# Performance work log

Measured on AMD Instinct MI355X. Metric: run time of the kernel, lower is better.

Reference implementation:

```python
import jax, jax.numpy as jnp
import numpy as np

N, E, B = 100000, 200000, 4096
D, FEAT, L = 300, 512, 5
NUM_ATOM, NUM_CHI = 119, 3
NUM_BOND, NUM_DIR = 5, 3
EPS = 1e-5


def setup_inputs() -> dict:
    key = jax.random.key(0)
    ks = jax.random.split(key, 24)
    x = jax.random.randint(ks[0], (N, 2), 0, 3, dtype=jnp.int32)
    edge_index = jax.random.randint(ks[1], (2, E), 0, N, dtype=jnp.int32)
    edge_attr = jax.random.randint(ks[2], (E, 2), 0, 3, dtype=jnp.int32)
    batch = jnp.sort(jax.random.randint(ks[3], (N,), 0, B, dtype=jnp.int32))
    s = 0.02
    p = {
        'x_emb1': jax.random.normal(ks[4], (NUM_ATOM, D)) * s,
        'x_emb2': jax.random.normal(ks[5], (NUM_CHI, D)) * s,
        'edge_emb1': jax.random.normal(ks[6], (L, NUM_BOND, D)) * s,
        'edge_emb2': jax.random.normal(ks[7], (L, NUM_DIR, D)) * s,
        'W1': jax.random.normal(ks[8], (L, D, 2 * D)) * s,
        'b1': jnp.zeros((L, 2 * D)),
        'W2': jax.random.normal(ks[9], (L, 2 * D, D)) * s,
        'b2': jnp.zeros((L, D)),
        'gamma': jnp.ones((L, D)),
        'beta': jnp.zeros((L, D)),
        'W_feat': jax.random.normal(ks[10], (D, FEAT)) * s,
        'b_feat': jnp.zeros((FEAT,)),
        'Wp1': jax.random.normal(ks[11], (FEAT, FEAT // 2)) * s,
        'bp1': jnp.zeros((FEAT // 2,)),
        'Wp2': jax.random.normal(ks[12], (FEAT // 2, FEAT // 2)) * s,
        'bp2': jnp.zeros((FEAT // 2,)),
        'Wp3': jax.random.normal(ks[13], (FEAT // 2, 2)) * s,
        'bp3': jnp.zeros((2,)),
    }
    return dict(x=x, edge_index=edge_index, edge_attr=edge_attr, batch=batch, **p)


def reference(x, edge_index, edge_attr, batch, x_emb1, x_emb2, edge_emb1, edge_emb2,
              W1, b1, W2, b2, gamma, beta, W_feat, b_feat, Wp1, bp1, Wp2, bp2, Wp3, bp3):
    n = x.shape[0]
    ar = jnp.arange(n, dtype=edge_index.dtype)
    src = jnp.concatenate([edge_index[0], ar])  # [E+N] message sources
    dst = jnp.concatenate([edge_index[1], ar])  # [E+N] aggregation targets
    # self-loop edge attr: bond type 4, direction 0
    sl = jnp.stack([jnp.full((n,), 4, edge_attr.dtype), jnp.zeros((n,), edge_attr.dtype)], axis=1)
    ea = jnp.concatenate([edge_attr, sl], axis=0)  # [E+N, 2]

    h = x_emb1[x[:, 0]] + x_emb2[x[:, 1]]  # [N, D]
    for l in range(L):
        ee = edge_emb1[l][ea[:, 0]] + edge_emb2[l][ea[:, 1]]  # [E+N, D]
        msg = h[src] + ee
        aggr = jax.ops.segment_sum(msg, dst, num_segments=n)  # GIN add-aggregate
        h = jax.nn.relu(aggr @ W1[l] + b1[l]) @ W2[l] + b2[l]
        mu = h.mean(axis=0)
        var = ((h - mu) ** 2).mean(axis=0)  # biased var (torch BN training mode)
        h = (h - mu) * jax.lax.rsqrt(var + EPS) * gamma[l] + beta[l]
        if l < L - 1:
            h = jax.nn.relu(h)

    ones = jnp.ones((n,), h.dtype)
    counts = jax.ops.segment_sum(ones, batch, num_segments=B)
    pooled = jax.ops.segment_sum(h, batch, num_segments=B) / jnp.maximum(counts, 1.0)[:, None]
    hf = pooled @ W_feat + b_feat  # [B, FEAT]
    p = jax.nn.softplus(hf @ Wp1 + bp1)
    p = jax.nn.softplus(p @ Wp2 + bp2)
    pred = p @ Wp3 + bp3  # [B, 2]
    return hf, pred
```

## Files before the change

### kernel.cpp

```cpp
#include <hip/hip_runtime.h>
#include <cstdint>
#include <cstddef>

typedef unsigned short u16;
typedef __bf16 bf16x8 __attribute__((ext_vector_type(8)));
typedef float  f32x4  __attribute__((ext_vector_type(4)));

#define NN 100000
#define EE 200000
#define BG 4096
#define DV 300
#define DP 320
#define D2 600
#define D2P 640
#define FEAT 512
#define FH 256
#define NL 5
#define CHUNK 50048
#define QN (NN/4)

__device__ __forceinline__ float b2f(u16 u) {
    union { float f; unsigned int i; } x; x.i = ((unsigned int)u) << 16; return x.f;
}
__device__ __forceinline__ u16 f2b(float f) {
    union { float f; unsigned int i; } x; x.f = f;
    unsigned int r = (x.i + 0x7FFFu + ((x.i >> 16) & 1u)) >> 16;
    return (u16)r;
}
__device__ __forceinline__ float ldp(const void* p, size_t i, int m) {
    return m ? ((const float*)p)[i] : b2f(((const u16*)p)[i]);
}

__global__ void detect_kernel(const void* w1raw, int* mode) {
    if (threadIdx.x != 0 || blockIdx.x != 0) return;
    const u16* p = (const u16*)w1raw;
    int cnt = 0;
    for (int i = 0; i < 128; ++i) {
        u16 v = p[2 * i];
        int e = (v >> 7) & 0xFF;
        if (e >= 100 && e <= 135) ++cnt;
    }
    *mode = (cnt >= 100) ? 0 : 1;
}

__global__ void zero_int_kernel(int* __restrict__ p, long n) {
    long i = (long)blockIdx.x * blockDim.x + threadIdx.x;
    long stride = (long)gridDim.x * blockDim.x;
    for (; i < n; i += stride) p[i] = 0;
}

__global__ void zero_stats_kernel(float* __restrict__ a, float* __restrict__ b) {
    int t = threadIdx.x; a[t] = 0.f; b[t] = 0.f;
}

__global__ void pack_kernel(const void* __restrict__ W1, const void* __restrict__ W2,
                            const void* __restrict__ Wf, const void* __restrict__ Wp1,
                            const void* __restrict__ Wp2,
                            const void* __restrict__ b1, const void* __restrict__ b2,
                            const void* __restrict__ bfe, const void* __restrict__ bp1,
                            const void* __restrict__ bp2,
                            u16* __restrict__ W1pT, u16* __restrict__ W2pT,
                            u16* __restrict__ WfT, u16* __restrict__ Wp1T, u16* __restrict__ Wp2T,
                            float* __restrict__ b1p, float* __restrict__ b2p,
                            float* __restrict__ bfp, float* __restrict__ bp1p, float* __restrict__ bp2p,
                            const int* __restrict__ modep)
{
    const int m = *modep;
    const int s1 = NL*D2P*DP, s2 = NL*DP*D2P, s3 = FEAT*DP, s4 = FH*FEAT, s5 = FH*FH;
    const int s6 = NL*D2P, s7 = NL*DP, s8 = FEAT, s9 = FH, s10 = FH;
    int idx = blockIdx.x * 256 + threadIdx.x;
    if (idx < s1) {
        int l = idx / (D2P*DP), r = idx % (D2P*DP), n = r / DP, k = r % DP;
        u16 v = 0;
        if (n < D2) {
            if (k < DV) v = f2b(ldp(W1, ((size_t)l*DV + k)*D2 + n, m));
            else if (k < DV + 8) return;
        }
        W1pT[idx] = v; return;
    } idx -= s1;
    if (idx < s2) {
        int l = idx / (DP*D2P), r = idx % (DP*D2P), n = r / D2P, k = r % D2P;
        W2pT[idx] = (n < DV && k < D2) ? f2b(ldp(W2, ((size_t)l*D2 + k)*DV + n, m)) : (u16)0; return;
    } idx -= s2;
    if (idx < s3) { int n = idx / DP, k = idx % DP;
        WfT[idx] = (k < DV) ? f2b(ldp(Wf, (size_t)k*FEAT + n, m)) : (u16)0; return; } idx -= s3;
    if (idx < s4) { int n = idx / FEAT, k = idx % FEAT;
        Wp1T[idx] = f2b(ldp(Wp1, (size_t)k*FH + n, m)); return; } idx -= s4;
    if (idx < s5) { int n = idx / FH, k = idx % FH;
        Wp2T[idx] = f2b(ldp(Wp2, (size_t)k*FH + n, m)); return; } idx -= s5;
    if (idx < s6) { int l = idx / D2P, n = idx % D2P;
        b1p[idx] = (n < D2) ? ldp(b1, l*D2 + n, m) : 0.f; return; } idx -= s6;
    if (idx < s7) { int l = idx / DP, n = idx % DP;
        b2p[idx] = (n < DV) ? ldp(b2, l*DV + n, m) : 0.f; return; } idx -= s7;
    if (idx < s8) { bfp[idx] = ldp(bfe, idx, m); return; } idx -= s8;
    if (idx < s9) { bp1p[idx] = ldp(bp1, idx, m); return; } idx -= s9;
    if (idx < s10) { bp2p[idx] = ldp(bp2, idx, m); return; }
}

__global__ void fold_kernel(const void* __restrict__ W1,
                            const void* __restrict__ eemb1, const void* __restrict__ eemb2,
                            u16* __restrict__ W1pT, const int* __restrict__ modep)
{
    const int m = *modep;
    __shared__ float e[DV];
    int b = blockIdx.x;
    int l = b >> 3, bin = b & 7;
    int n = threadIdx.x;
    for (int d = n; d < DV; d += 640)
        e[d] = (bin < 5) ? ldp(eemb1, ((size_t)l*5 + bin)*DV + d, m)
                         : ldp(eemb2, ((size_t)l*3 + (bin-5))*DV + d, m);
    __syncthreads();
    if (n >= D2) return;
    float acc = 0.f;
    for (int d = 0; d < DV; ++d)
        acc += e[d] * ldp(W1, ((size_t)l*DV + d)*D2 + n, m);
    W1pT[((size_t)l*D2P + n)*DP + DV + bin] = f2b(acc);
}

__global__ void count_kernel(const int* __restrict__ ei, const int* __restrict__ ea,
                             int* __restrict__ indeg, int* __restrict__ cnt)
{
    int e = blockIdx.x * 256 + threadIdx.x;
    if (e >= EE) return;
    int dst = ei[EE + e];
    atomicAdd(&indeg[dst], 1);
    atomicAdd(&cnt[dst*8 + ea[e*2]], 1);
    atomicAdd(&cnt[dst*8 + 5 + ea[e*2+1]], 1);
}

__global__ void scan1_kernel(const int* __restrict__ in, int* __restrict__ out,
                             int* __restrict__ partials, int n)
{
    __shared__ int sm[256];
    int t = threadIdx.x, gi = blockIdx.x * 256 + t;
    int v = (gi < n) ? in[gi] : 0;
    sm[t] = v; __syncthreads();
    int acc = v;
    for (int off = 1; off < 256; off <<= 1) {
        int other = (t >= off) ? sm[t - off] : 0;
        __syncthreads();
        acc += other; sm[t] = acc;
        __syncthreads();
    }
    if (gi < n) out[gi] = acc - v;
    if (t == 255) partials[blockIdx.x] = acc;
}

__global__ void scan2_kernel(int* __restrict__ partials, int nb)
{
    __shared__ int sm[512];
    int t = threadIdx.x;
    int v = (t < nb) ? partials[t] : 0;
    sm[t] = v; __syncthreads();
    int acc = v;
    for (int off = 1; off < 512; off <<= 1) {
        int other = (t >= off) ? sm[t - off] : 0;
        __syncthreads();
        acc += other; sm[t] = acc;
        __syncthreads();
    }
    if (t < nb) partials[t] = acc - v;
}

__global__ void scan3_kernel(int* __restrict__ rowptr, const int* __restrict__ partials,
                             int* __restrict__ cursor, int n)
{
    int i = blockIdx.x * 256 + threadIdx.x;
    if (i < n) {
        int v = rowptr[i] + partials[i >> 8];
        rowptr[i] = v; cursor[i] = v;
    }
    if (i == n) rowptr[n] = EE;
}

__global__ void fill_kernel(const int* __restrict__ ei, int* __restrict__ cursor,
                            int* __restrict__ colidx)
{
    int e = blockIdx.x * 256 + threadIdx.x;
    if (e >= EE) return;
    int src = ei[e], dst = ei[EE + e];
    int pos = atomicAdd(&cursor[dst], 1);
    colidx[pos] = src;
}

__global__ void h0_kernel(const int* __restrict__ x, const void* __restrict__ e1,
                          const void* __restrict__ e2, u16* __restrict__ H,
                          const int* __restrict__ modep)
{
    const int m = *modep;
    int i = blockIdx.x, d = threadIdx.x;
    u16 r = 0;
    if (d < DV) {
        int a = x[i*2], b = x[i*2+1];
        r = f2b(ldp(e1, (size_t)a*DV + d, m) + ldp(e2, (size_t)b*DV + d, m));
    }
    H[(size_t)i*DP + d] = r;
}

template<bool BN>
__global__ __launch_bounds__(320)
void aggr_kernel(const u16* __restrict__ H, const int* __restrict__ rowptr,
                 const int* __restrict__ colidx, const int* __restrict__ cnt,
                 const float* __restrict__ sc, const float* __restrict__ sh,
                 u16* __restrict__ out)
{
    const int b = blockIdx.x, d = threadIdx.x;
    int node[4];
    #pragma unroll
    for (int k = 0; k < 4; ++k) node[k] = b + k * QN;

    if (d < DV) {
        float scv = BN ? sc[d] : 1.f, shv = BN ? sh[d] : 0.f;
        float acc[4];
        int e0[4], deg[4]; int maxdeg = 0;
        #pragma unroll
        for (int k = 0; k < 4; ++k) {
            e0[k] = rowptr[node[k]];
            deg[k] = rowptr[node[k] + 1] - e0[k];
            maxdeg = max(maxdeg, deg[k]);
            float h = b2f(H[(size_t)node[k]*DP + d]);
            if (BN) h = fmaxf(h * scv + shv, 0.f);
            acc[k] = h;
        }
        for (int j = 0; j < maxdeg; ++j) {
            int idx[4];
            #pragma unroll
            for (int k = 0; k < 4; ++k) {
                int jj = e0[k] + j; if (jj > EE - 1) jj = EE - 1;
                idx[k] = (j < deg[k]) ? colidx[jj] : node[k];
            }
            float hv[4];
            #pragma unroll
            for (int k = 0; k < 4; ++k) hv[k] = b2f(H[(size_t)idx[k]*DP + d]);
            #pragma unroll
            for (int k = 0; k < 4; ++k) {
                float h = hv[k];
                if (BN) h = fmaxf(h * scv + shv, 0.f);
                if (j < deg[k]) acc[k] += h;
            }
        }
        #pragma unroll
        for (int k = 0; k < 4; ++k) out[(size_t)node[k]*DP + d] = f2b(acc[k]);
    } else {
        #pragma unroll
        for (int k = 0; k < 4; ++k) {
            float v = 0.f;
            if (d < DV + 8) {
                int c = cnt[node[k]*8 + (d - DV)];
                if (d == DV + 4 || d == DV + 5) c += 1;
                v = (float)c;
            }
            out[(size_t)node[k]*DP + d] = f2b(v);
        }
    }
}

template<int EPI, bool F32OUT, bool STATS>
__global__ __launch_bounds__(256)
void gemm_bt(const u16* __restrict__ A, int lda,
             const u16* __restrict__ Bt,
             const float* __restrict__ bias,
             u16* __restrict__ C, float* __restrict__ Cf, int ldc,
             int M, int Ncols, int K,
             float* __restrict__ cs, float* __restrict__ cs2)
{
    const int MT = (M + 127) >> 7, NT = (Ncols + 127) >> 7;
    const int total = MT * NT;
    int id = blockIdx.x;
    int nper = (total + 7) >> 3;
    int slot = (id & 7) * nper + (id >> 3);
    if (slot >= total) return;
    const int m0 = (slot / NT) * 128;
    const int n0 = (slot % NT) * 128;

    __shared__ __align__(16) u16 As[128*64];
    __shared__ __align__(16) u16 Bs[128*64];
    const int t = threadIdx.x;
    const int w = t >> 6, l = t & 63;
    const int wm = (w & 1) * 64, wn = (w >> 1) * 64;
    const int srow = l >> 3;
    const int sg   = ((l & 7) ^ srow) * 8;
    const int fr = l & 15, q = l >> 4;

    f32x4 acc[4][4] = {};

    for (int k0 = 0; k0 < K; k0 += 64) {
        #pragma unroll
        for (int i = 0; i < 8; ++i) {
            int cc = w * 8 + i;
            int rl = (cc & 15) * 8 + srow;
            if (cc < 16) {
                int row = m0 + rl; if (row >= M) row = M - 1;
                const u16* gp = A + (size_t)row * lda + (k0 + sg);
                __builtin_amdgcn_global_load_lds((__attribute__((address_space(1))) void*)gp,
                                                 (__attribute__((address_space(3))) void*)(As + cc*512), 16, 0, 0);
            } else {
                int row = n0 + rl; if (row >= Ncols) row = Ncols - 1;
                const u16* gp = Bt + (size_t)row * K + (k0 + sg);
                __builtin_amdgcn_global_load_lds((__attribute__((address_space(1))) void*)gp,
                                                 (__attribute__((address_space(3))) void*)(Bs + (cc-16)*512), 16, 0, 0);
            }
        }
        asm volatile("s_waitcnt vmcnt(0)" ::: "memory");
        __syncthreads();

        #pragma unroll
        for (int s = 0; s < 2; ++s) {
            bf16x8 af[4], bv[4];
            #pragma unroll
            for (int mi = 0; mi < 4; ++mi) {
                int R = wm + mi*16 + fr;
                int g = (s*4 + q) ^ (R & 7);
                af[mi] = *reinterpret_cast<const bf16x8*>(As + R*64 + g*8);
            }
            #pragma unroll
            for (int ni = 0; ni < 4; ++ni) {
                int R = wn + ni*16 + fr;
                int g = (s*4 + q) ^ (R & 7);
                bv[ni] = *reinterpret_cast<const bf16x8*>(Bs + R*64 + g*8);
            }
            #pragma unroll
            for (int mi = 0; mi < 4; ++mi)
                #pragma unroll
                for (int ni = 0; ni < 4; ++ni)
                    acc[mi][ni] = __builtin_amdgcn_mfma_f32_16x16x32_bf16(af[mi], bv[ni], acc[mi][ni], 0, 0, 0);
        }
        __syncthreads();
    }

    const int orow = q * 4, ocol = l & 15;
    #pragma unroll
    for (int ni = 0; ni < 4; ++ni) {
        int col = n0 + wn + ni*16 + ocol;
        if (col >= Ncols) continue;
        float bvv = bias[col];
        float s = 0.f, s2 = 0.f;
        #pragma unroll
        for (int mi = 0; mi < 4; ++mi) {
            #pragma unroll
            for (int r = 0; r < 4; ++r) {
                int row = m0 + wm + mi*16 + orow + r;
                if (row < M) {
                    float v = acc[mi][ni][r] + bvv;
                    if (EPI == 1) v = fmaxf(v, 0.f);
                    else if (EPI == 2) v = fmaxf(v, 0.f) + log1pf(expf(-fabsf(v)));
                    C[(size_t)row * ldc + col] = f2b(v);
                    if (F32OUT) Cf[(size_t)row * ldc + col] = v;
                    if (STATS) { s += v; s2 += v * v; }
                }
            }
        }
        if (STATS) {
            s  += __shfl_xor(s, 16);  s  += __shfl_xor(s, 32);
            s2 += __shfl_xor(s2, 16); s2 += __shfl_xor(s2, 32);
            if (q == 0) {
                atomicAdd(&cs[col], s);
                atomicAdd(&cs2[col], s2);
            }
        }
    }
}

__global__ void bn_finalize(const float* __restrict__ cs, const float* __restrict__ cs2,
                            const void* __restrict__ gamma, const void* __restrict__ beta,
                            int goff, float* __restrict__ sc, float* __restrict__ sh,
                            const int* __restrict__ modep)
{
    const int m = *modep;
    int d = threadIdx.x;
    float a = 0.f, bb = 0.f;
    if (d < DV) {
        float mu = cs[d] / (float)NN;
        float var = cs2[d] / (float)NN - mu * mu;
        var = fmaxf(var, 0.f);
        a = ldp(gamma, goff + d, m) * rsqrtf(var + 1e-5f);
        bb = ldp(beta, goff + d, m) - mu * a;
    }
    sc[d] = a; sh[d] = bb;
}

__global__ void gstart_kernel(const int* __restrict__ batch, int* __restrict__ gs)
{
    int i = blockIdx.x * 256 + threadIdx.x;
    if (i >= NN) return;
    int b = batch[i];
    int pb = (i == 0) ? -1 : batch[i-1];
    for (int g = pb + 1; g <= b; ++g) gs[g] = i;
    if (i == NN - 1) for (int g = b + 1; g <= BG; ++g) gs[g] = NN;
}

__global__ __launch_bounds__(256)
void pool_kernel(const u16* __restrict__ H, const int* __restrict__ gs,
                 const float* __restrict__ sc, const float* __restrict__ sh,
                 u16* __restrict__ pooled)
{
    __shared__ float red[4][320];
    int b = blockIdx.x;
    int wv = threadIdx.x >> 6, lane = threadIdx.x & 63;
    int s = gs[b], e = gs[b+1];
    if (lane < 40) {
        int d0 = lane * 8;
        float a[8] = {0.f,0.f,0.f,0.f,0.f,0.f,0.f,0.f};
        for (int r = s + wv; r < e; r += 4) {
            uint4 row = *(const uint4*)(H + (size_t)r * DP + d0);
            const u16* p = (const u16*)&row;
            #pragma unroll
            for (int j = 0; j < 8; ++j) a[j] += b2f(p[j]);
        }
        #pragma unroll
        for (int j = 0; j < 8; ++j) red[wv][d0 + j] = a[j];
    }
    __syncthreads();
    if (wv == 0 && lane < 40) {
        int d0 = lane * 8;
        int c = e - s; if (c < 1) c = 1;
        float inv = 1.f / (float)c;
        union { uint4 v; u16 o[8]; } pk;
        #pragma unroll
        for (int j = 0; j < 8; ++j) {
            int d = d0 + j;
            float m = (red[0][d] + red[1][d] + red[2][d] + red[3][d]) * inv;
            pk.o[j] = f2b(m * sc[d] + sh[d]);
        }
        *(uint4*)(pooled + (size_t)b * DP + d0) = pk.v;
    }
}

__global__ void pred_kernel(const u16* __restrict__ P2, const void* __restrict__ W3,
                            const void* __restrict__ b3, float* __restrict__ out,
                            const int* __restrict__ modep)
{
    const int m = *modep;
    int r = blockIdx.x, l = threadIdx.x;
    float a0 = 0.f, a1 = 0.f;
    for (int k = l; k < FH; k += 64) {
        float p = b2f(P2[(size_t)r*FH + k]);
        a0 += p * ldp(W3, k*2, m);
        a1 += p * ldp(W3, k*2 + 1, m);
    }
    for (int o = 32; o > 0; o >>= 1) {
        a0 += __shfl_down(a0, o);
        a1 += __shfl_down(a1, o);
    }
    if (l == 0) {
        out[(size_t)r*2]     = a0 + ldp(b3, 0, m);
        out[(size_t)r*2 + 1] = a1 + ldp(b3, 1, m);
    }
}

static inline int gemm_grid(int M, int Ncols) {
    int total = ((M + 127) / 128) * ((Ncols + 127) / 128);
    return ((total + 7) / 8) * 8;
}

extern "C" void kernel_launch(void* const* d_in, const int* in_sizes, int n_in,
                              void* d_out, int out_size, void* d_ws, size_t ws_size,
                              hipStream_t stream)
{
    const int* x      = (const int*)d_in[0];
    const int* ei     = (const int*)d_in[1];
    const int* ea     = (const int*)d_in[2];
    const int* batch  = (const int*)d_in[3];
    const void* x_emb1 = d_in[4];
    const void* x_emb2 = d_in[5];
    const void* eemb1  = d_in[6];
    const void* eemb2  = d_in[7];
    const void* W1     = d_in[8];
    const void* b1     = d_in[9];
    const void* W2     = d_in[10];
    const void* b2     = d_in[11];
    const void* gamma  = d_in[12];
    const void* beta   = d_in[13];
    const void* Wf     = d_in[14];
    const void* bfe    = d_in[15];
    const void* Wp1    = d_in[16];
    const void* bp1    = d_in[17];
    const void* Wp2    = d_in[18];
    const void* bp2    = d_in[19];
    const void* Wp3    = d_in[20];
    const void* bp3    = d_in[21];
    float* outf = (float*)d_out;

    char* ws = (char*)d_ws;
    size_t off = 0;
    auto carve = [&](size_t bytes) -> char* {
        size_t a = (off + 255) & ~(size_t)255; off = a + bytes; return ws + a;
    };

    u16* H      = (u16*)carve((size_t)NN * DP * 2);
    u16* AGGR   = (u16*)carve((size_t)NN * DP * 2);
    u16* T      = (u16*)carve((size_t)CHUNK * D2P * 2);
    u16* POOLED = (u16*)carve((size_t)BG * DP * 2);
    u16* HFB    = (u16*)carve((size_t)BG * FEAT * 2);
    u16* P1     = (u16*)carve((size_t)BG * FH * 2);
    u16* P2     = (u16*)carve((size_t)BG * FH * 2);
    u16* W1pT   = (u16*)carve((size_t)NL * D2P * DP * 2);
    u16* W2pT   = (u16*)carve((size_t)NL * DP * D2P * 2);
    u16* WfT    = (u16*)carve((size_t)FEAT * DP * 2);
    u16* Wp1T   = (u16*)carve((size_t)FH * FEAT * 2);
    u16* Wp2T   = (u16*)carve((size_t)FH * FH * 2);
    float* B1P  = (float*)carve((size_t)NL * D2P * 4);
    float* B2P  = (float*)carve((size_t)NL * DP * 4);
    float* BFP  = (float*)carve((size_t)FEAT * 4);
    float* BP1P = (float*)carve((size_t)FH * 4);
    float* BP2P = (float*)carve((size_t)FH * 4);
    int* INDEG  = (int*)carve((size_t)9 * NN * 4);
    int* CNT    = INDEG + NN;
    int* ROWPTR = (int*)carve((size_t)(NN + 1) * 4);
    int* CURSOR = (int*)carve((size_t)NN * 4);
    int* COLIDX = (int*)carve((size_t)EE * 4);
    int* PART   = (int*)carve(512 * 4);
    float* CS   = (float*)carve(DP * 4);
    float* CS2  = (float*)carve(DP * 4);
    float* BNSC = (float*)carve((size_t)NL * DP * 4);
    float* BNSH = (float*)carve((size_t)NL * DP * 4);
    int* GS     = (int*)carve((size_t)(BG + 1) * 4);
    int* MODEP  = (int*)carve(4);
    (void)ws_size; (void)in_sizes; (void)n_in; (void)out_size;

    detect_kernel<<<1, 64, 0, stream>>>(W1, MODEP);

    const int PACK_TOTAL = NL*D2P*DP + NL*DP*D2P + FEAT*DP + FH*FEAT + FH*FH
                         + NL*D2P + NL*DP + FEAT + FH + FH;
    pack_kernel<<<(PACK_TOTAL + 255)/256, 256, 0, stream>>>(
        W1, W2, Wf, Wp1, Wp2, b1, b2, bfe, bp1, bp2,
        W1pT, W2pT, WfT, Wp1T, Wp2T, B1P, B2P, BFP, BP1P, BP2P, MODEP);
    fold_kernel<<<NL*8, 640, 0, stream>>>(W1, eemb1, eemb2, W1pT, MODEP);

    zero_int_kernel<<<2048, 256, 0, stream>>>(INDEG, (long)9 * NN);
    count_kernel<<<(EE + 255)/256, 256, 0, stream>>>(ei, ea, INDEG, CNT);

    const int NB = (NN + 255) / 256;
    scan1_kernel<<<NB, 256, 0, stream>>>(INDEG, ROWPTR, PART, NN);
    scan2_kernel<<<1, 512, 0, stream>>>(PART, NB);
    scan3_kernel<<<(NN + 256)/256, 256, 0, stream>>>(ROWPTR, PART, CURSOR, NN);
    fill_kernel<<<(EE + 255)/256, 256, 0, stream>>>(ei, CURSOR, COLIDX);

    h0_kernel<<<NN, DP, 0, stream>>>(x, x_emb1, x_emb2, H, MODEP);
    gstart_kernel<<<(NN + 255)/256, 256, 0, stream>>>(batch, GS);

    for (int l = 0; l < NL; ++l) {
        if (l == 0)
            aggr_kernel<false><<<QN, DP, 0, stream>>>(H, ROWPTR, COLIDX, CNT,
                                                      nullptr, nullptr, AGGR);
        else
            aggr_kernel<true><<<QN, DP, 0, stream>>>(H, ROWPTR, COLIDX, CNT,
                                                     BNSC + (l-1)*DP, BNSH + (l-1)*DP, AGGR);
        zero_stats_kernel<<<1, DP, 0, stream>>>(CS, CS2);
        for (int r0 = 0; r0 < NN; r0 += CHUNK) {
            int mc = NN - r0; if (mc > CHUNK) mc = CHUNK;
            gemm_bt<1,false,false><<<gemm_grid(mc, D2P), 256, 0, stream>>>(
                AGGR + (size_t)r0*DP, DP, W1pT + (size_t)l*D2P*DP,
                B1P + l*D2P, T, nullptr, D2P, mc, D2P, DP, nullptr, nullptr);
            gemm_bt<0,false,true><<<gemm_grid(mc, DP), 256, 0, stream>>>(
                T, D2P, W2pT + (size_t)l*DP*D2P,
                B2P + l*DP, H + (size_t)r0*DP, nullptr, DP, mc, DP, D2P, CS, CS2);
        }
        bn_finalize<<<1, DP, 0, stream>>>(CS, CS2, gamma, beta, l*DV,
                                          BNSC + l*DP, BNSH + l*DP, MODEP);
    }

    pool_kernel<<<BG, 256, 0, stream>>>(H, GS, BNSC + 4*DP, BNSH + 4*DP, POOLED);
    gemm_bt<0,true,false><<<gemm_grid(BG, FEAT), 256, 0, stream>>>(
        POOLED, DP, WfT, BFP, HFB, outf, FEAT, BG, FEAT, DP, nullptr, nullptr);
    gemm_bt<2,false,false><<<gemm_grid(BG, FH), 256, 0, stream>>>(
        HFB, FEAT, Wp1T, BP1P, P1, nullptr, FH, BG, FH, FEAT, nullptr, nullptr);
    gemm_bt<2,false,false><<<gemm_grid(BG, FH), 256, 0, stream>>>(
        P1, FH, Wp2T, BP2P, P2, nullptr, FH, BG, FH, FH, nullptr, nullptr);
    pred_kernel<<<BG, 64, 0, stream>>>(P2, Wp3, bp3, outf + (size_t)BG*FEAT, MODEP);
}
```

Before: 1.860 ms.

## Stage GEMM epilogue through LDS for vector stores, widen aggregation batching

The GEMM epilogue now writes bf16 results into shared memory in two passes and then emits coalesced 16-byte global stores, replacing scattered 2-byte stores. The aggregation kernel processes 8 nodes per block instead of 4, giving more gathers in flight per thread at the cost of more registers and fewer blocks. BN statistics are now reset inside bn_finalize, which removes one zero_stats launch per layer. The LDS staging adds two extra barriers per tile and reuses the As buffer.

```diff
diff --git a/kernel.cpp b/kernel.cpp
--- a/kernel.cpp
+++ b/kernel.cpp
@@ -17,7 +17,7 @@
 #define FH 256
 #define NL 5
 #define CHUNK 50048
-#define QN (NN/4)
+#define QN (NN/8)
 
 __device__ __forceinline__ float b2f(u16 u) {
     union { float f; unsigned int i; } x; x.i = ((unsigned int)u) << 16; return x.f;
@@ -205,16 +205,16 @@
                  u16* __restrict__ out)
 {
     const int b = blockIdx.x, d = threadIdx.x;
-    int node[4];
+    int node[8];
     #pragma unroll
-    for (int k = 0; k < 4; ++k) node[k] = b + k * QN;
+    for (int k = 0; k < 8; ++k) node[k] = b + k * QN;
 
     if (d < DV) {
         float scv = BN ? sc[d] : 1.f, shv = BN ? sh[d] : 0.f;
-        float acc[4];
-        int e0[4], deg[4]; int maxdeg = 0;
-        #pragma unroll
-        for (int k = 0; k < 4; ++k) {
+        float acc[8];
+        int e0[8], deg[8]; int maxdeg = 0;
+        #pragma unroll
+        for (int k = 0; k < 8; ++k) {
             e0[k] = rowptr[node[k]];
             deg[k] = rowptr[node[k] + 1] - e0[k];
             maxdeg = max(maxdeg, deg[k]);
@@ -223,27 +223,27 @@
             acc[k] = h;
         }
         for (int j = 0; j < maxdeg; ++j) {
-            int idx[4];
-            #pragma unroll
-            for (int k = 0; k < 4; ++k) {
+            int idx[8];
+            #pragma unroll
+            for (int k = 0; k < 8; ++k) {
                 int jj = e0[k] + j; if (jj > EE - 1) jj = EE - 1;
                 idx[k] = (j < deg[k]) ? colidx[jj] : node[k];
             }
-            float hv[4];
-            #pragma unroll
-            for (int k = 0; k < 4; ++k) hv[k] = b2f(H[(size_t)idx[k]*DP + d]);
-            #pragma unroll
-            for (int k = 0; k < 4; ++k) {
+            float hv[8];
+            #pragma unroll
+            for (int k = 0; k < 8; ++k) hv[k] = b2f(H[(size_t)idx[k]*DP + d]);
+            #pragma unroll
+            for (int k = 0; k < 8; ++k) {
                 float h = hv[k];
                 if (BN) h = fmaxf(h * scv + shv, 0.f);
                 if (j < deg[k]) acc[k] += h;
             }
         }
         #pragma unroll
-        for (int k = 0; k < 4; ++k) out[(size_t)node[k]*DP + d] = f2b(acc[k]);
+        for (int k = 0; k < 8; ++k) out[(size_t)node[k]*DP + d] = f2b(acc[k]);
     } else {
         #pragma unroll
-        for (int k = 0; k < 4; ++k) {
+        for (int k = 0; k < 8; ++k) {
             float v = 0.f;
             if (d < DV + 8) {
                 int c = cnt[node[k]*8 + (d - DV)];
@@ -332,46 +332,94 @@
     #pragma unroll
     for (int ni = 0; ni < 4; ++ni) {
         int col = n0 + wn + ni*16 + ocol;
-        if (col >= Ncols) continue;
-        float bvv = bias[col];
+        float bvv = (col < Ncols) ? bias[col] : 0.f;
         float s = 0.f, s2 = 0.f;
         #pragma unroll
         for (int mi = 0; mi < 4; ++mi) {
             #pragma unroll
             for (int r = 0; r < 4; ++r) {
-                int row = m0 + wm + mi*16 + orow + r;
-                if (row < M) {
-                    float v = acc[mi][ni][r] + bvv;
-                    if (EPI == 1) v = fmaxf(v, 0.f);
-                    else if (EPI == 2) v = fmaxf(v, 0.f) + log1pf(expf(-fabsf(v)));
-                    C[(size_t)row * ldc + col] = f2b(v);
-                    if (F32OUT) Cf[(size_t)row * ldc + col] = v;
-                    if (STATS) { s += v; s2 += v * v; }
+                float v = acc[mi][ni][r] + bvv;
+                if (EPI == 1) v = fmaxf(v, 0.f);
+                else if (EPI == 2) v = fmaxf(v, 0.f) + log1pf(expf(-fabsf(v)));
+                acc[mi][ni][r] = v;
+                if (STATS) {
+                    int row = m0 + wm + mi*16 + orow + r;
+                    if (row < M && col < Ncols) { s += v; s2 += v * v; }
                 }
             }
         }
         if (STATS) {
             s  += __shfl_xor(s, 16);  s  += __shfl_xor(s, 32);
             s2 += __shfl_xor(s2, 16); s2 += __shfl_xor(s2, 32);
-            if (q == 0) {
+            if (q == 0 && col < Ncols) {
                 atomicAdd(&cs[col], s);
                 atomicAdd(&cs2[col], s2);
             }
         }
     }
-}
-
-__global__ void bn_finalize(const float* __restrict__ cs, const float* __restrict__ cs2,
+
+    if (!F32OUT) {
+        #pragma unroll
+        for (int p = 0; p < 2; ++p) {
+            if ((w & 1) == p) {
+                #pragma unroll
+                for (int mi = 0; mi < 4; ++mi)
+                    #pragma unroll
+                    for (int ni = 0; ni < 4; ++ni)
+                        #pragma unroll
+                        for (int r = 0; r < 4; ++r) {
+                            int lr = mi*16 + q*4 + r;
+                            int lc = wn + ni*16 + ocol;
+                            int slc = (lc + q*16) & 127;
+                            As[lr*128 + slc] = f2b(acc[mi][ni][r]);
+                        }
+            }
+            __syncthreads();
+            #pragma unroll
+            for (int j = 0; j < 4; ++j) {
+                int u = t*4 + j;
+                int lr = u >> 4, lc8 = (u & 15) * 8;
+                int slc = (lc8 + ((lr >> 2) & 3) * 16) & 127;
+                int grow = m0 + p*64 + lr, gcol = n0 + lc8;
+                if (grow < M && gcol < Ncols)
+                    *(uint4*)(C + (size_t)grow*ldc + gcol) = *(const uint4*)(As + lr*128 + slc);
+            }
+            __syncthreads();
+        }
+    } else {
+        #pragma unroll
+        for (int ni = 0; ni < 4; ++ni) {
+            int col = n0 + wn + ni*16 + ocol;
+            if (col >= Ncols) continue;
+            #pragma unroll
+            for (int mi = 0; mi < 4; ++mi) {
+                #pragma unroll
+                for (int r = 0; r < 4; ++r) {
+                    int row = m0 + wm + mi*16 + orow + r;
+                    if (row < M) {
+                        float v = acc[mi][ni][r];
+                        C[(size_t)row * ldc + col] = f2b(v);
+                        Cf[(size_t)row * ldc + col] = v;
+                    }
+                }
+            }
+        }
+    }
+}
+
+__global__ void bn_finalize(float* __restrict__ cs, float* __restrict__ cs2,
                             const void* __restrict__ gamma, const void* __restrict__ beta,
                             int goff, float* __restrict__ sc, float* __restrict__ sh,
                             const int* __restrict__ modep)
 {
     const int m = *modep;
     int d = threadIdx.x;
+    float s = cs[d], s2 = cs2[d];
+    cs[d] = 0.f; cs2[d] = 0.f;
     float a = 0.f, bb = 0.f;
     if (d < DV) {
-        float mu = cs[d] / (float)NN;
-        float var = cs2[d] / (float)NN - mu * mu;
+        float mu = s / (float)NN;
+        float var = s2 / (float)NN - mu * mu;
         var = fmaxf(var, 0.f);
         a = ldp(gamma, goff + d, m) * rsqrtf(var + 1e-5f);
         bb = ldp(beta, goff + d, m) - mu * a;
@@ -528,6 +576,7 @@
     fold_kernel<<<NL*8, 640, 0, stream>>>(W1, eemb1, eemb2, W1pT, MODEP);
 
     zero_int_kernel<<<2048, 256, 0, stream>>>(INDEG, (long)9 * NN);
+    zero_stats_kernel<<<1, DP, 0, stream>>>(CS, CS2);
     count_kernel<<<(EE + 255)/256, 256, 0, stream>>>(ei, ea, INDEG, CNT);
 
     const int NB = (NN + 255) / 256;
@@ -546,7 +595,6 @@
         else
             aggr_kernel<true><<<QN, DP, 0, stream>>>(H, ROWPTR, COLIDX, CNT,
                                                      BNSC + (l-1)*DP, BNSH + (l-1)*DP, AGGR);
-        zero_stats_kernel<<<1, DP, 0, stream>>>(CS, CS2);
         for (int r0 = 0; r0 < NN; r0 += CHUNK) {
             int mc = NN - r0; if (mc > CHUNK) mc = CHUNK;
             gemm_bt<1,false,false><<<gemm_grid(mc, D2P), 256, 0, stream>>>(
```

Result: faster. 1.636 ms, median of 2 (-12.0%).
